# Kernel tuning notes

Hardware: AMD Instinct MI355X
Metric: run time of the kernel (lower is better)

## Reference

```python
import jax, jax.numpy as jnp
import numpy as np

B, T, E, H = 4, 2048, 1024, 2048  # note: T must equal H (mask shape constraint in source)


def setup_inputs() -> dict:
    key = jax.random.key(0)
    ks = jax.random.split(key, 5)
    x = jax.random.normal(ks[0], (B, T, E), dtype=jnp.float32)
    Wq = jax.random.normal(ks[1], (E, H), dtype=jnp.float32) * 0.02
    bq = jnp.zeros((H,), dtype=jnp.float32)
    Wv = jax.random.normal(ks[2], (E, H), dtype=jnp.float32) * 0.02
    bv = jnp.zeros((H,), dtype=jnp.float32)
    return {"x": x, "Wq": Wq, "bq": bq, "Wv": Wv, "bv": bv}


def reference(x, Wq, bq, Wv, bv):
    # NOTE: original code uses q_proj for BOTH q and k (k = self.q_proj(x)),
    # so k is identical to q; k_proj params are dead. We reproduce that.
    q = x @ Wq + bq                                  # [B, T, H]
    v = x @ Wv + bv                                  # [B, T, H]
    scores = jnp.einsum('bqd,bkd->bqk', q, q)        # q @ k.mT with k == q
    scaled = scores / jnp.sqrt(jnp.float32(Wq.shape[1]))
    mask = jnp.tril(jnp.ones((scaled.shape[1], scaled.shape[2]), dtype=scaled.dtype))
    masked = scaled * mask                           # multiplicative mask (as in source)
    attn = jax.nn.softmax(masked, axis=1)            # softmax over dim=1 (query axis), as in source
    return attn @ v                                  # [B, T, H]
```

## Files before the change

kernel.cpp:

```cpp
#include <hip/hip_runtime.h>


#define B_DIM 4
#define T_DIM 2048
#define E_DIM 1024
#define H_DIM 2048

typedef __attribute__((ext_vector_type(8))) short bf16x8;
typedef __attribute__((ext_vector_type(4))) short s16x4;
typedef __attribute__((ext_vector_type(4))) float f32x4;

__device__ __forceinline__ float bf2f(short s) {
  union { float f; unsigned u; } x; x.u = ((unsigned)(unsigned short)s) << 16; return x.f;
}
__device__ __forceinline__ short f2bf(float f) {
  union { float f; unsigned u; } x; x.f = f;
  unsigned r = x.u + 0x7fff + ((x.u >> 16) & 1);
  return (short)(r >> 16);
}

__device__ __forceinline__ void gload16(const short* g, short* l) {
  __builtin_amdgcn_global_load_lds(
      (const __attribute__((address_space(1))) void*)g,
      (__attribute__((address_space(3))) void*)l, 16, 0, 0);
}

template<int MODE>
__global__ __launch_bounds__(256) void gemm_bt(
    const short* __restrict__ Ag, const short* __restrict__ Bg,
    const float* __restrict__ bias, const float* __restrict__ bias2,
    void* __restrict__ Cg, void* __restrict__ Cg2,
    float* __restrict__ colsum, const float* __restrict__ sfx,
    int M, int N, int K, long sA, long sB, long sC, float scale)
{
  __shared__ __align__(16) short As[128 * 64];
  __shared__ __align__(16) short Bs[128 * 64];
  __shared__ float csum[128];

  const int t = threadIdx.x;
  const int bz = blockIdx.z;

  int rt, ct;
  if (MODE == 1) {
    int idx = 135 - blockIdx.x;
    rt = (int)((sqrtf(8.0f * idx + 1.0f) - 1.0f) * 0.5f);
    while ((rt + 1) * (rt + 2) / 2 <= idx) rt++;
    while (rt * (rt + 1) / 2 > idx) rt--;
    ct = idx - rt * (rt + 1) / 2;
  } else if (MODE == 2) {
    rt = (gridDim.x - 1) - blockIdx.x;
    ct = blockIdx.y;
  } else {
    rt = blockIdx.y; ct = blockIdx.x;
  }

  const short* A = Ag + (long)bz * sA + (long)rt * 128 * K;
  const short* B = Bg + (long)bz * sB + (long)ct * 128 * K;
  const int kEnd = (MODE == 2) ? (rt + 1) * 128 : K;

  const int lane = t & 63;
  const int wave = t >> 6;
  const int wr = wave >> 1, wc = wave & 1;
  const int l16 = lane & 15, kg = lane >> 4;

  if (MODE == 1) { if (t < 128) csum[t] = 0.0f; }

  f32x4 acc[4][4] = {};

  for (int k0 = 0; k0 < kEnd; k0 += 64) {
    __syncthreads();
#pragma unroll
    for (int j = 0; j < 4; ++j) {
      const int e = j * 256 + t;
      const int r = e >> 3, cl = e & 7;
      const int cg = cl ^ (r & 7);
      gload16(A + (long)r * K + (k0 + cg * 8), &As[e * 8]);
      gload16(B + (long)r * K + (k0 + cg * 8), &Bs[e * 8]);
    }
    __syncthreads();
#pragma unroll
    for (int kk = 0; kk < 2; ++kk) {
      bf16x8 af[4], bfr[4];
#pragma unroll
      for (int mi = 0; mi < 4; ++mi)
        af[mi] = *(const bf16x8*)&As[(wr * 64 + mi * 16 + l16) * 64 +
                                     ((kk * 4 + kg) ^ (l16 & 7)) * 8];
#pragma unroll
      for (int ni = 0; ni < 4; ++ni)
        bfr[ni] = *(const bf16x8*)&Bs[(wc * 64 + ni * 16 + l16) * 64 +
                                      ((kk * 4 + kg) ^ (l16 & 7)) * 8];
#pragma unroll
      for (int mi = 0; mi < 4; ++mi)
#pragma unroll
        for (int ni = 0; ni < 4; ++ni)
          acc[mi][ni] = __builtin_amdgcn_mfma_f32_16x16x32_bf16(af[mi], bfr[ni], acc[mi][ni], 0, 0, 0);
    }
  }

  const int rowb = rt * 128 + wr * 64 + kg * 4;
  const int colb = ct * 128 + wc * 64 + l16;

  if (MODE == 1) {
    short* C = (short*)Cg + (long)bz * sC;
    float ps[4] = {0.f, 0.f, 0.f, 0.f};
#pragma unroll
    for (int mi = 0; mi < 4; ++mi)
#pragma unroll
      for (int ni = 0; ni < 4; ++ni)
#pragma unroll
        for (int r = 0; r < 4; ++r) {
          int row = rowb + mi * 16 + r;
          int col = colb + ni * 16;
          float e = (row >= col) ? __expf(acc[mi][ni][r] * scale) : 1.0f;
          C[(long)row * N + col] = f2bf(e);
          ps[ni] += e;
        }
#pragma unroll
    for (int ni = 0; ni < 4; ++ni)
      atomicAdd(&csum[wc * 64 + ni * 16 + l16], ps[ni]);
    __syncthreads();
    if (t < 128)
      atomicAdd(&colsum[(long)bz * N + ct * 128 + t], csum[t]);
  } else if (MODE == 0) {
    const int Nh = N >> 1;
#pragma unroll
    for (int mi = 0; mi < 4; ++mi)
#pragma unroll
      for (int ni = 0; ni < 4; ++ni) {
        int col = colb + ni * 16;
        short* C = (col < Nh) ? (short*)Cg : (short*)Cg2;
        const float* bp = (col < Nh) ? bias : bias2;
        int c2 = col & (Nh - 1);
        float bv = bp[c2];
#pragma unroll
        for (int r = 0; r < 4; ++r) {
          int row = rowb + mi * 16 + r;
          C[(long)row * Nh + c2] = f2bf(acc[mi][ni][r] + bv);
        }
      }
  } else {
    float* C = (float*)Cg + (long)bz * sC;
    const float* sf = sfx + ((long)bz * 16 + rt) * N;
#pragma unroll
    for (int mi = 0; mi < 4; ++mi)
#pragma unroll
      for (int ni = 0; ni < 4; ++ni) {
        int col = colb + ni * 16;
        float s = sf[col];
#pragma unroll
        for (int r = 0; r < 4; ++r) {
          int row = rowb + mi * 16 + r;
          C[(long)row * N + col] = acc[mi][ni][r] + s;
        }
      }
  }
}

__global__ __launch_bounds__(256) void f32_to_bf16(
    const float* __restrict__ src, short* __restrict__ dst, long n)
{
  long i = ((long)blockIdx.x * blockDim.x + threadIdx.x) * 4;
  if (i < n) {
    const float4 v = *(const float4*)(src + i);
    s16x4 o;
    o.x = f2bf(v.x); o.y = f2bf(v.y); o.z = f2bf(v.z); o.w = f2bf(v.w);
    *(s16x4*)(dst + i) = o;
  }
}

template<bool IN_F32>
__global__ __launch_bounds__(256) void transpose_scale(
    const void* __restrict__ src_, short* __restrict__ dst,
    const float* __restrict__ sums, int R, int Cn, long sSrc, long sDst, long sSum)
{
  __shared__ short tile[64][65];
  const int t = threadIdx.x;
  const int c0 = blockIdx.x * 64;
  const int r0 = blockIdx.y * 64;
  const int bz = blockIdx.z;
  short* d = dst + (long)bz * sDst;
  const int cx = t & 63, ry = t >> 6;
#pragma unroll
  for (int i = 0; i < 16; ++i) {
    int r = ry + i * 4;
    float v;
    if (IN_F32)
      v = ((const float*)src_ + (long)bz * sSrc)[(long)(r0 + r) * Cn + c0 + cx];
    else
      v = bf2f(((const short*)src_ + (long)bz * sSrc)[(long)(r0 + r) * Cn + c0 + cx]);
    if (sums) v *= 1.0f / sums[(long)bz * sSum + r0 + r];
    tile[r][cx] = f2bf(v);
  }
  __syncthreads();
#pragma unroll
  for (int i = 0; i < 16; ++i) {
    int rr = ry + i * 4;
    d[(long)(c0 + rr) * R + r0 + cx] = tile[cx][rr];
  }
}

__global__ __launch_bounds__(256) void colsum_init(float* __restrict__ colsum)
{
  int i = blockIdx.x * 256 + threadIdx.x;
  int k = i & (T_DIM - 1);
  colsum[i] = 128.0f * (float)(k >> 7);
}

__global__ __launch_bounds__(256) void block_psum(
    const short* __restrict__ v, const float* __restrict__ colsum,
    float* __restrict__ psum)
{
  const int h = blockIdx.x * 256 + threadIdx.x;
  const int j = blockIdx.y, bz = blockIdx.z;
  const short* vb = v + (long)bz * T_DIM * H_DIM;
  const float* cs = colsum + (long)bz * T_DIM;
  float s = 0.f;
  const int k0 = j * 128;
  for (int k = k0; k < k0 + 128; ++k)
    s += bf2f(vb[(long)k * H_DIM + h]) * (1.0f / cs[k]);
  psum[((long)bz * 16 + j) * H_DIM + h] = s;
}

__global__ __launch_bounds__(256) void suffix_scan(
    const float* __restrict__ psum, float* __restrict__ sfx)
{
  const int h = blockIdx.x * 256 + threadIdx.x;
  const int bz = blockIdx.z;
  const long base = (long)bz * 16 * H_DIM + h;
  float suf = 0.f;
  sfx[base + 15L * H_DIM] = 0.f;
  for (int j = 15; j >= 1; --j) {
    suf += psum[base + (long)j * H_DIM];
    sfx[base + (long)(j - 1) * H_DIM] = suf;
  }
}

extern "C" void kernel_launch(void* const* d_in, const int* in_sizes, int n_in,
                              void* d_out, int out_size, void* d_ws, size_t ws_size,
                              hipStream_t stream) {
  const float* x  = (const float*)d_in[0];
  const float* Wq = (const float*)d_in[1];
  const float* bq = (const float*)d_in[2];
  const float* Wv = (const float*)d_in[3];
  const float* bv = (const float*)d_in[4];
  float* out = (float*)d_out;

  char* ws = (char*)d_ws;
  short* P      = (short*)(ws);
  short* q      = (short*)(ws + (size_t)32 * 1024 * 1024);
  short* v      = (short*)(ws + (size_t)64 * 1024 * 1024);
  float* colsum = (float*)(ws + (size_t)96 * 1024 * 1024);
  float* sfx    = (float*)(ws + (size_t)96 * 1024 * 1024 + 32 * 1024);
  short* vT = q;

  short* xb    = (short*)d_out;
  short* WqvT  = (short*)((char*)d_out + (size_t)16 * 1024 * 1024);
  float* psum  = (float*)((char*)d_out + (size_t)24 * 1024 * 1024);

  const float scale = 0.022097086912079612f;
  dim3 blk(256);

  f32_to_bf16<<<dim3((B_DIM * T_DIM * E_DIM) / (256 * 4)), blk, 0, stream>>>(
      x, xb, (long)B_DIM * T_DIM * E_DIM);
  transpose_scale<true><<<dim3(H_DIM / 64, E_DIM / 64, 1), blk, 0, stream>>>(
      Wq, WqvT, nullptr, E_DIM, H_DIM, 0, 0, 0);
  transpose_scale<true><<<dim3(H_DIM / 64, E_DIM / 64, 1), blk, 0, stream>>>(
      Wv, WqvT + (size_t)H_DIM * E_DIM, nullptr, E_DIM, H_DIM, 0, 0, 0);

  gemm_bt<0><<<dim3((2 * H_DIM) / 128, (B_DIM * T_DIM) / 128, 1), blk, 0, stream>>>(
      xb, WqvT, bq, bv, q, v, nullptr, nullptr,
      B_DIM * T_DIM, 2 * H_DIM, E_DIM, 0, 0, 0, 1.f);

  colsum_init<<<dim3((B_DIM * T_DIM) / 256), blk, 0, stream>>>(colsum);

  gemm_bt<1><<<dim3(136, 1, B_DIM), blk, 0, stream>>>(
      q, q, nullptr, nullptr, P, nullptr, colsum, nullptr, T_DIM, T_DIM, H_DIM,
      (long)T_DIM * H_DIM, (long)T_DIM * H_DIM, (long)T_DIM * T_DIM, scale);

  transpose_scale<false><<<dim3(H_DIM / 64, T_DIM / 64, B_DIM), blk, 0, stream>>>(
      v, vT, colsum, T_DIM, H_DIM, (long)T_DIM * H_DIM, (long)H_DIM * T_DIM, T_DIM);

  block_psum<<<dim3(H_DIM / 256, 16, B_DIM), blk, 0, stream>>>(v, colsum, psum);
  suffix_scan<<<dim3(H_DIM / 256, 1, B_DIM), blk, 0, stream>>>(psum, sfx);

  gemm_bt<2><<<dim3(T_DIM / 128, H_DIM / 128, B_DIM), blk, 0, stream>>>(
      P, vT, nullptr, nullptr, out, nullptr, nullptr, sfx, T_DIM, H_DIM, T_DIM,
      (long)T_DIM * T_DIM, (long)H_DIM * T_DIM, (long)T_DIM * H_DIM, 1.f);
}
```

Measured before the change: 387.9 us.

## Stage GEMM epilogues through LDS for vectorized stores and streamline auxiliary kernels

The MODE 0 and MODE 1 GEMM epilogues now write results into the shared LDS buffer, then store them to global memory as 16-byte vectors per row instead of scattered 2-byte writes. The weight transposes are merged into one launch with float4 loads. The V transpose-scale and block_psum kernels now use vectorized loads and stores. The colsum init kernel is replaced by a memset, with the diagonal-tile offset folded into the MODE 1 csum initialisation. This targets uncoalesced stores and launch overhead, at the cost of extra LDS traffic and barriers in the epilogues.

```diff
diff --git a/kernel.cpp b/kernel.cpp
--- a/kernel.cpp
+++ b/kernel.cpp
@@ -33,8 +33,9 @@
     float* __restrict__ colsum, const float* __restrict__ sfx,
     int M, int N, int K, long sA, long sB, long sC, float scale)
 {
-  __shared__ __align__(16) short As[128 * 64];
-  __shared__ __align__(16) short Bs[128 * 64];
+  __shared__ __align__(16) short lds[128 * 64 * 2];
+  short* As = lds;
+  short* Bs = lds + 128 * 64;
   __shared__ float csum[128];
 
   const int t = threadIdx.x;
@@ -63,7 +64,7 @@
   const int wr = wave >> 1, wc = wave & 1;
   const int l16 = lane & 15, kg = lane >> 4;
 
-  if (MODE == 1) { if (t < 128) csum[t] = 0.0f; }
+  if (MODE == 1) { if (t < 128) csum[t] = (rt == ct) ? 128.0f * ct : 0.0f; }
 
   f32x4 acc[4][4] = {};
 
@@ -97,48 +98,65 @@
     }
   }
 
-  const int rowb = rt * 128 + wr * 64 + kg * 4;
-  const int colb = ct * 128 + wc * 64 + l16;
-
   if (MODE == 1) {
-    short* C = (short*)Cg + (long)bz * sC;
+    short* Cs = lds;
+    __syncthreads();
     float ps[4] = {0.f, 0.f, 0.f, 0.f};
 #pragma unroll
     for (int mi = 0; mi < 4; ++mi)
 #pragma unroll
-      for (int ni = 0; ni < 4; ++ni)
+      for (int ni = 0; ni < 4; ++ni) {
+        const int cl = wc * 64 + ni * 16 + l16;
+        const int col = ct * 128 + cl;
 #pragma unroll
         for (int r = 0; r < 4; ++r) {
-          int row = rowb + mi * 16 + r;
-          int col = colb + ni * 16;
+          const int rl = wr * 64 + kg * 4 + mi * 16 + r;
+          const int row = rt * 128 + rl;
           float e = (row >= col) ? __expf(acc[mi][ni][r] * scale) : 1.0f;
-          C[(long)row * N + col] = f2bf(e);
+          Cs[rl * 128 + cl] = f2bf(e);
           ps[ni] += e;
         }
+      }
 #pragma unroll
     for (int ni = 0; ni < 4; ++ni)
       atomicAdd(&csum[wc * 64 + ni * 16 + l16], ps[ni]);
     __syncthreads();
+    short* C = (short*)Cg + (long)bz * sC;
+    const int rr = t >> 1, cc = (t & 1) * 64;
+    const long gbase = (long)(rt * 128 + rr) * N + ct * 128 + cc;
+#pragma unroll
+    for (int j = 0; j < 8; ++j)
+      *(bf16x8*)(C + gbase + j * 8) = *(const bf16x8*)&Cs[rr * 128 + cc + j * 8];
     if (t < 128)
       atomicAdd(&colsum[(long)bz * N + ct * 128 + t], csum[t]);
   } else if (MODE == 0) {
+    short* Cs = lds;
+    __syncthreads();
     const int Nh = N >> 1;
 #pragma unroll
     for (int mi = 0; mi < 4; ++mi)
 #pragma unroll
       for (int ni = 0; ni < 4; ++ni) {
-        int col = colb + ni * 16;
-        short* C = (col < Nh) ? (short*)Cg : (short*)Cg2;
-        const float* bp = (col < Nh) ? bias : bias2;
-        int c2 = col & (Nh - 1);
-        float bv = bp[c2];
+        const int cl = wc * 64 + ni * 16 + l16;
+        const int colg = ct * 128 + cl;
+        const float bv = (colg < Nh) ? bias[colg] : bias2[colg - Nh];
 #pragma unroll
         for (int r = 0; r < 4; ++r) {
-          int row = rowb + mi * 16 + r;
-          C[(long)row * Nh + c2] = f2bf(acc[mi][ni][r] + bv);
+          const int rl = wr * 64 + kg * 4 + mi * 16 + r;
+          Cs[rl * 128 + cl] = f2bf(acc[mi][ni][r] + bv);
         }
       }
+    __syncthreads();
+    short* C = (ct * 128 < Nh) ? (short*)Cg : (short*)Cg2;
+    const int colofs = (ct * 128) & (Nh - 1);
+    const int rr = t >> 1, cc = (t & 1) * 64;
+    const long gbase = (long)(rt * 128 + rr) * Nh + colofs + cc;
+#pragma unroll
+    for (int j = 0; j < 8; ++j)
+      *(bf16x8*)(C + gbase + j * 8) = *(const bf16x8*)&Cs[rr * 128 + cc + j * 8];
   } else {
+    const int rowb = rt * 128 + wr * 64 + kg * 4;
+    const int colb = ct * 128 + wc * 64 + l16;
     float* C = (float*)Cg + (long)bz * sC;
     const float* sf = sfx + ((long)bz * 16 + rt) * N;
 #pragma unroll
@@ -168,57 +186,86 @@
   }
 }
 
-template<bool IN_F32>
-__global__ __launch_bounds__(256) void transpose_scale(
-    const void* __restrict__ src_, short* __restrict__ dst,
-    const float* __restrict__ sums, int R, int Cn, long sSrc, long sDst, long sSum)
+__global__ __launch_bounds__(256) void wtrans(
+    const float* __restrict__ src0, const float* __restrict__ src1,
+    short* __restrict__ dst)
+{
+  __shared__ short tile[64][65];
+  const int t = threadIdx.x;
+  const int c0 = blockIdx.x * 64;
+  const int r0 = blockIdx.y * 64;
+  const float* s = blockIdx.z ? src1 : src0;
+  short* d = dst + (long)blockIdx.z * H_DIM * E_DIM;
+  const int rl = t >> 4, cb = (t & 15) * 4;
+#pragma unroll
+  for (int i = 0; i < 4; ++i) {
+    int r = rl + i * 16;
+    const float4 w = *(const float4*)(s + (long)(r0 + r) * H_DIM + c0 + cb);
+    tile[r][cb + 0] = f2bf(w.x); tile[r][cb + 1] = f2bf(w.y);
+    tile[r][cb + 2] = f2bf(w.z); tile[r][cb + 3] = f2bf(w.w);
+  }
+  __syncthreads();
+#pragma unroll
+  for (int i = 0; i < 4; ++i) {
+    int rr = rl + i * 16;
+    s16x4 o;
+    o.x = tile[cb + 0][rr]; o.y = tile[cb + 1][rr];
+    o.z = tile[cb + 2][rr]; o.w = tile[cb + 3][rr];
+    *(s16x4*)(d + (long)(c0 + rr) * E_DIM + r0 + cb) = o;
+  }
+}
+
+__global__ __launch_bounds__(256) void vtrans(
+    const short* __restrict__ src, short* __restrict__ dst,
+    const float* __restrict__ sums)
 {
   __shared__ short tile[64][65];
   const int t = threadIdx.x;
   const int c0 = blockIdx.x * 64;
   const int r0 = blockIdx.y * 64;
   const int bz = blockIdx.z;
-  short* d = dst + (long)bz * sDst;
-  const int cx = t & 63, ry = t >> 6;
-#pragma unroll
-  for (int i = 0; i < 16; ++i) {
-    int r = ry + i * 4;
-    float v;
-    if (IN_F32)
-      v = ((const float*)src_ + (long)bz * sSrc)[(long)(r0 + r) * Cn + c0 + cx];
-    else
-      v = bf2f(((const short*)src_ + (long)bz * sSrc)[(long)(r0 + r) * Cn + c0 + cx]);
-    if (sums) v *= 1.0f / sums[(long)bz * sSum + r0 + r];
-    tile[r][cx] = f2bf(v);
+  const short* s = src + (long)bz * T_DIM * H_DIM;
+  short* d = dst + (long)bz * H_DIM * T_DIM;
+  const float* su = sums + (long)bz * T_DIM;
+  const int rl = t >> 4, cb = (t & 15) * 4;
+#pragma unroll
+  for (int i = 0; i < 4; ++i) {
+    int r = rl + i * 16;
+    const float rs = 1.0f / su[r0 + r];
+    const s16x4 w = *(const s16x4*)(s + (long)(r0 + r) * H_DIM + c0 + cb);
+    tile[r][cb + 0] = f2bf(bf2f(w.x) * rs); tile[r][cb + 1] = f2bf(bf2f(w.y) * rs);
+    tile[r][cb + 2] = f2bf(bf2f(w.z) * rs); tile[r][cb + 3] = f2bf(bf2f(w.w) * rs);
   }
   __syncthreads();
 #pragma unroll
-  for (int i = 0; i < 16; ++i) {
-    int rr = ry + i * 4;
-    d[(long)(c0 + rr) * R + r0 + cx] = tile[cx][rr];
-  }
-}
-
-__global__ __launch_bounds__(256) void colsum_init(float* __restrict__ colsum)
-{
-  int i = blockIdx.x * 256 + threadIdx.x;
-  int k = i & (T_DIM - 1);
-  colsum[i] = 128.0f * (float)(k >> 7);
+  for (int i = 0; i < 4; ++i) {
+    int rr = rl + i * 16;
+    s16x4 o;
+    o.x = tile[cb + 0][rr]; o.y = tile[cb + 1][rr];
+    o.z = tile[cb + 2][rr]; o.w = tile[cb + 3][rr];
+    *(s16x4*)(d + (long)(c0 + rr) * T_DIM + r0 + cb) = o;
+  }
 }
 
 __global__ __launch_bounds__(256) void block_psum(
     const short* __restrict__ v, const float* __restrict__ colsum,
     float* __restrict__ psum)
 {
-  const int h = blockIdx.x * 256 + threadIdx.x;
+  const int h = (blockIdx.x * 256 + threadIdx.x) * 2;
   const int j = blockIdx.y, bz = blockIdx.z;
   const short* vb = v + (long)bz * T_DIM * H_DIM;
   const float* cs = colsum + (long)bz * T_DIM;
-  float s = 0.f;
+  float s0 = 0.f, s1 = 0.f;
   const int k0 = j * 128;
-  for (int k = k0; k < k0 + 128; ++k)
-    s += bf2f(vb[(long)k * H_DIM + h]) * (1.0f / cs[k]);
-  psum[((long)bz * 16 + j) * H_DIM + h] = s;
+  for (int k = k0; k < k0 + 128; ++k) {
+    union { int i; short s[2]; } w;
+    w.i = *(const int*)(vb + (long)k * H_DIM + h);
+    const float rs = 1.0f / cs[k];
+    s0 += bf2f(w.s[0]) * rs;
+    s1 += bf2f(w.s[1]) * rs;
+  }
+  float* p = psum + ((long)bz * 16 + j) * H_DIM + h;
+  p[0] = s0; p[1] = s1;
 }
 
 __global__ __launch_bounds__(256) void suffix_scan(
@@ -260,27 +307,22 @@
   const float scale = 0.022097086912079612f;
   dim3 blk(256);
 
+  hipMemsetAsync(colsum, 0, (size_t)B_DIM * T_DIM * 4, stream);
+
   f32_to_bf16<<<dim3((B_DIM * T_DIM * E_DIM) / (256 * 4)), blk, 0, stream>>>(
       x, xb, (long)B_DIM * T_DIM * E_DIM);
-  transpose_scale<true><<<dim3(H_DIM / 64, E_DIM / 64, 1), blk, 0, stream>>>(
-      Wq, WqvT, nullptr, E_DIM, H_DIM, 0, 0, 0);
-  transpose_scale<true><<<dim3(H_DIM / 64, E_DIM / 64, 1), blk, 0, stream>>>(
-      Wv, WqvT + (size_t)H_DIM * E_DIM, nullptr, E_DIM, H_DIM, 0, 0, 0);
+  wtrans<<<dim3(H_DIM / 64, E_DIM / 64, 2), blk, 0, stream>>>(Wq, Wv, WqvT);
 
   gemm_bt<0><<<dim3((2 * H_DIM) / 128, (B_DIM * T_DIM) / 128, 1), blk, 0, stream>>>(
       xb, WqvT, bq, bv, q, v, nullptr, nullptr,
       B_DIM * T_DIM, 2 * H_DIM, E_DIM, 0, 0, 0, 1.f);
 
-  colsum_init<<<dim3((B_DIM * T_DIM) / 256), blk, 0, stream>>>(colsum);
-
   gemm_bt<1><<<dim3(136, 1, B_DIM), blk, 0, stream>>>(
       q, q, nullptr, nullptr, P, nullptr, colsum, nullptr, T_DIM, T_DIM, H_DIM,
       (long)T_DIM * H_DIM, (long)T_DIM * H_DIM, (long)T_DIM * T_DIM, scale);
 
-  transpose_scale<false><<<dim3(H_DIM / 64, T_DIM / 64, B_DIM), blk, 0, stream>>>(
-      v, vT, colsum, T_DIM, H_DIM, (long)T_DIM * H_DIM, (long)H_DIM * T_DIM, T_DIM);
-
-  block_psum<<<dim3(H_DIM / 256, 16, B_DIM), blk, 0, stream>>>(v, colsum, psum);
+  vtrans<<<dim3(H_DIM / 64, T_DIM / 64, B_DIM), blk, 0, stream>>>(v, vT, colsum);
+  block_psum<<<dim3(H_DIM / 512, 16, B_DIM), blk, 0, stream>>>(v, colsum, psum);
   suffix_scan<<<dim3(H_DIM / 256, 1, B_DIM), blk, 0, stream>>>(psum, sfx);
 
   gemm_bt<2><<<dim3(T_DIM / 128, H_DIM / 128, B_DIM), blk, 0, stream>>>(
```

After: 371.5 us. 4.2% less time.
